# Optimization experiments

Measured on AMD Instinct MI355X. Metric: run time of the kernel, lower is better.

## Reference

```python
import jax, jax.numpy as jnp
import numpy as np

N = 100000   # nodes
E = 1600000  # edges (before self-loops)
F = 128      # num_features
H = 128      # hidden_dim
EPS = 1e-5   # BatchNorm eps


def setup_inputs() -> dict:
    key = jax.random.key(0)
    ks = jax.random.split(key, 8)
    x = jax.random.normal(ks[0], (N, F), dtype=jnp.float32)
    edge_index = jax.random.randint(ks[1], (2, E), 0, N, dtype=jnp.int64)

    def lin(k, din, dout):
        s = 1.0 / np.sqrt(din)
        kw, kb = jax.random.split(k)
        W = jax.random.uniform(kw, (din, dout), jnp.float32, -s, s)
        b = jax.random.uniform(kb, (dout,), jnp.float32, -s, s)
        return W, b

    W1, b1 = lin(ks[2], F, H)
    W2, b2 = lin(ks[3], H, H)
    W3, b3 = lin(ks[4], H, H)
    Wc, bc = lin(ks[5], H, 2)

    def bn_params():
        return (jnp.ones((H,), jnp.float32), jnp.zeros((H,), jnp.float32),
                jnp.zeros((H,), jnp.float32), jnp.ones((H,), jnp.float32))

    g1, be1, rm1, rv1 = bn_params()
    g2, be2, rm2, rv2 = bn_params()
    g3, be3, rm3, rv3 = bn_params()

    return {"x": x, "edge_index": edge_index,
            "W1": W1, "b1": b1, "W2": W2, "b2": b2, "W3": W3, "b3": b3,
            "g1": g1, "be1": be1, "rm1": rm1, "rv1": rv1,
            "g2": g2, "be2": be2, "rm2": rm2, "rv2": rv2,
            "g3": g3, "be3": be3, "rm3": rm3, "rv3": rv3,
            "Wc": Wc, "bc": bc}


def _gcn_norm(edge_index, num_nodes):
    # add self-loops, compute symmetric normalization (PyG GCNConv default)
    loop = jnp.arange(num_nodes, dtype=edge_index.dtype)
    src = jnp.concatenate([edge_index[0], loop])
    dst = jnp.concatenate([edge_index[1], loop])
    deg = jax.ops.segment_sum(jnp.ones_like(dst, dtype=jnp.float32), dst,
                              num_segments=num_nodes)
    dinv = jnp.where(deg > 0, jax.lax.rsqrt(deg), 0.0)
    norm = dinv[src] * dinv[dst]  # [E+N]
    return src, dst, norm


def _gcn_conv(x, W, b, src, dst, norm, num_nodes):
    h = x @ W                              # [N, H] linear first
    msg = h[src] * norm[:, None]           # gather + scale  [E+N, H]
    out = jax.ops.segment_sum(msg, dst, num_segments=num_nodes)  # scatter-add
    return out + b


def _bn_eval(x, g, be, rm, rv):
    return (x - rm) * jax.lax.rsqrt(rv + EPS) * g + be


def reference(x, edge_index,
              W1, b1, W2, b2, W3, b3,
              g1, be1, rm1, rv1,
              g2, be2, rm2, rv2,
              g3, be3, rm3, rv3,
              Wc, bc):
    n = x.shape[0]
    src, dst, norm = _gcn_norm(edge_index, n)
    h = _gcn_conv(x, W1, b1, src, dst, norm, n)
    h = _bn_eval(jax.nn.relu(h), g1, be1, rm1, rv1)
    # dropout: identity in eval mode
    h = _gcn_conv(h, W2, b2, src, dst, norm, n)
    h = _bn_eval(jax.nn.relu(h), g2, be2, rm2, rv2)
    h = _gcn_conv(h, W3, b3, src, dst, norm, n)
    h = _bn_eval(jax.nn.relu(h), g3, be3, rm3, rv3)
    return h @ Wc + bc  # [N, 2]
```

## Files before the change

### kernel.cpp

```cpp
#include <hip/hip_runtime.h>
#include <hip/hip_fp16.h>

#define BN_EPS 1e-5f
#define CHUNK 4096
#define BBITS 7

typedef _Float16 half8 __attribute__((ext_vector_type(8)));
typedef float f32x4 __attribute__((ext_vector_type(4)));

__device__ __forceinline__ float4 f4zero() { return make_float4(0.f, 0.f, 0.f, 0.f); }


__global__ __launch_bounds__(256) void k_pack_hist(const float* __restrict__ W1,
                                                   const float* __restrict__ W2,
                                                   const float* __restrict__ W3,
                                                   _Float16* __restrict__ pW,
                                                   const int* __restrict__ dst,
                                                   int* __restrict__ tableT,
                                                   int nA, int nbuck, int e) {
    __shared__ int h[1024];
    int tid = threadIdx.x;
    if (blockIdx.x < 24) {
        int t = blockIdx.x * 256 + tid;
        int wi = t >> 11;
        int tt = t & 2047;
        const float* W = (wi == 0) ? W1 : ((wi == 1) ? W2 : W3);
        int kc = tt >> 9;
        int rem = tt & 511;
        int ct = rem >> 6;
        int lane = rem & 63;
        int q = lane >> 4;
        int col = ct * 16 + (lane & 15);
        half8 hh;
#pragma unroll
        for (int j = 0; j < 8; ++j)
            hh[j] = (_Float16)W[(kc * 32 + q * 8 + j) * 128 + col];
        *(half8*)(pW + (size_t)t * 8) = hh;
        return;
    }
    int blk = blockIdx.x - 24;
    for (int k = tid; k < 1024; k += 256) h[k] = 0;
    __syncthreads();
    int base = blk * CHUNK;
    if (base + CHUNK <= e && (e & 3) == 0) {
        const int4* d4 = (const int4*)(dst + base);
#pragma unroll
        for (int t = 0; t < CHUNK / 1024; ++t) {
            int4 d = d4[t * 256 + tid];
            atomicAdd(&h[d.x >> BBITS], 1);
            atomicAdd(&h[d.y >> BBITS], 1);
            atomicAdd(&h[d.z >> BBITS], 1);
            atomicAdd(&h[d.w >> BBITS], 1);
        }
    } else {
        for (int i = base + tid; i < e && i < base + CHUNK; i += 256)
            atomicAdd(&h[dst[i] >> BBITS], 1);
    }
    __syncthreads();
    for (int k = tid; k < nbuck; k += 256)
        tableT[(size_t)k * nA + blk] = h[k];
}


__global__ __launch_bounds__(1024) void k_scan_block(const int* __restrict__ in,
                                                     int* __restrict__ outp,
                                                     int* __restrict__ partials, int len) {
    __shared__ int s[1024];
    int t = threadIdx.x;
    int gid = blockIdx.x * 1024 + t;
    int v = (gid < len) ? in[gid] : 0;
    int x = v;
    s[t] = x;
    __syncthreads();
    for (int d = 1; d < 1024; d <<= 1) {
        int y = (t >= d) ? s[t - d] : 0;
        __syncthreads();
        x += y;
        s[t] = x;
        __syncthreads();
    }
    if (gid < len) outp[gid] = x - v;
    if (t == 1023) partials[blockIdx.x] = x;
}

__global__ __launch_bounds__(256) void k_scan_addp(int* __restrict__ data,
                                                   const int* __restrict__ partials, int len) {
    __shared__ int red[256];
    int tid = threadIdx.x;
    int K = blockIdx.x >> 2;
    int s = 0;
    for (int t = tid; t < K; t += 256) s += partials[t];
    red[tid] = s;
    __syncthreads();
    for (int d = 128; d > 0; d >>= 1) {
        if (tid < d) red[tid] += red[tid + d];
        __syncthreads();
    }
    int gid = blockIdx.x * 256 + tid;
    if (gid < len) data[gid] += red[0];
}


template <bool AF32>
__device__ __forceinline__ void gemm_body(int bid, int tid, char* smem,
                                          const void* __restrict__ Av,
                                          const _Float16* __restrict__ pW,
                                          uint4* __restrict__ C, int n) {
    uint4* sW = (uint4*)smem;
    {
        const uint4* gW = (const uint4*)pW;
#pragma unroll
        for (int i = 0; i < 8; ++i) sW[tid + 256 * i] = gW[tid + 256 * i];
    }
    __syncthreads();

    int wave = tid >> 6, lane = tid & 63;
    int quad = lane >> 4, l16 = lane & 15;
    int row0 = bid * 64 + wave * 16;
    int arow = row0 + l16;
    int arowc = (arow < n) ? arow : (n - 1);

    half8 af[4];
    if (AF32) {
        const float* A = (const float*)Av + (size_t)arowc * 128 + quad * 8;
#pragma unroll
        for (int kc = 0; kc < 4; ++kc) {
            float4 lo = *(const float4*)(A + kc * 32);
            float4 hi = *(const float4*)(A + kc * 32 + 4);
            half8 h;
            h[0] = (_Float16)lo.x; h[1] = (_Float16)lo.y;
            h[2] = (_Float16)lo.z; h[3] = (_Float16)lo.w;
            h[4] = (_Float16)hi.x; h[5] = (_Float16)hi.y;
            h[6] = (_Float16)hi.z; h[7] = (_Float16)hi.w;
            af[kc] = h;
        }
    } else {
        const _Float16* A = (const _Float16*)Av + (size_t)arowc * 128 + quad * 8;
#pragma unroll
        for (int kc = 0; kc < 4; ++kc)
            af[kc] = *(const half8*)(A + kc * 32);
    }

    f32x4 acc[8];
#pragma unroll
    for (int ct = 0; ct < 8; ++ct) acc[ct] = (f32x4){0.f, 0.f, 0.f, 0.f};

#pragma unroll
    for (int kc = 0; kc < 4; ++kc) {
#pragma unroll
        for (int ct = 0; ct < 8; ++ct) {
            half8 bf = *(half8*)&sW[(kc * 8 + ct) * 64 + lane];
            acc[ct] = __builtin_amdgcn_mfma_f32_16x16x32_f16(af[kc], bf, acc[ct], 0, 0, 0);
        }
    }

    __syncthreads();

    _Float16* eb = (_Float16*)smem + wave * 16 * 136;
#pragma unroll
    for (int ct = 0; ct < 8; ++ct)
#pragma unroll
        for (int r = 0; r < 4; ++r)
            eb[(quad * 4 + r) * 136 + ct * 16 + l16] = (_Float16)(acc[ct][r]);

#pragma unroll
    for (int i = 0; i < 4; ++i) {
        int linear = i * 64 + lane;
        int r = linear >> 4, c = linear & 15;
        uint4 v = *(uint4*)((char*)eb + r * 272 + c * 16);
        int row = row0 + r;
        if (row < n) C[(size_t)row * 16 + c] = v;
    }
}

__global__ __launch_bounds__(256) void k_gemm_mfma(const void* __restrict__ Av,
                                                   const _Float16* __restrict__ pW,
                                                   uint4* __restrict__ C, int n) {
    __shared__ char smem[32768];
    gemm_body<false>(blockIdx.x, threadIdx.x, smem, Av, pW, C, n);
}


__global__ __launch_bounds__(256) void k_scatter_gemm(const int* __restrict__ src,
                                                      const int* __restrict__ dst,
                                                      const int* __restrict__ tableT,
                                                      int2* __restrict__ bed,
                                                      int nA, int nbuck, int e,
                                                      const float* __restrict__ x,
                                                      const _Float16* __restrict__ pW,
                                                      uint4* __restrict__ C, int n) {
    __shared__ char smem[32768];
    int tid = threadIdx.x;
    if ((int)blockIdx.x >= nA) {
        gemm_body<true>((int)blockIdx.x - nA, tid, smem, x, pW, C, n);
        return;
    }
    int* cur = (int*)smem;
    int blk = blockIdx.x;
    for (int k = tid; k < nbuck; k += 256)
        cur[k] = tableT[(size_t)k * nA + blk];
    __syncthreads();
    int base = blk * CHUNK;
    if (base + CHUNK <= e && (e & 3) == 0) {
        const int4* s4 = (const int4*)(src + base);
        const int4* d4 = (const int4*)(dst + base);
#pragma unroll
        for (int t = 0; t < CHUNK / 1024; ++t) {
            int4 s = s4[t * 256 + tid];
            int4 d = d4[t * 256 + tid];
            int p0 = atomicAdd(&cur[d.x >> BBITS], 1); bed[p0] = make_int2(s.x, d.x);
            int p1 = atomicAdd(&cur[d.y >> BBITS], 1); bed[p1] = make_int2(s.y, d.y);
            int p2 = atomicAdd(&cur[d.z >> BBITS], 1); bed[p2] = make_int2(s.z, d.z);
            int p3 = atomicAdd(&cur[d.w >> BBITS], 1); bed[p3] = make_int2(s.w, d.w);
        }
    } else {
        for (int i = base + tid; i < e && i < base + CHUNK; i += 256) {
            int d = dst[i];
            int p = atomicAdd(&cur[d >> BBITS], 1);
            bed[p] = make_int2(src[i], d);
        }
    }
}


__global__ __launch_bounds__(256) void k_rank_finalize(const int2* __restrict__ bed,
                                                       const int* __restrict__ tableT,
                                                       int2* __restrict__ offs2,
                                                       int* __restrict__ er,
                                                       float* __restrict__ dinv,
                                                       unsigned int* __restrict__ bufAzero,
                                                       int nA, int nbuck, int n, int e) {
    __shared__ int lcnt[128];
    __shared__ int lscan[128];
    __shared__ int loff[128];
    int b = blockIdx.x, tid = threadIdx.x;
    if (tid < 128) lcnt[tid] = 0;
    __syncthreads();
    int start = tableT[(size_t)b * nA];
    int end = (b + 1 < nbuck) ? tableT[(size_t)(b + 1) * nA] : e;
    for (int i = start + tid; i < end; i += 256)
        atomicAdd(&lcnt[bed[i].y & 127], 1);
    __syncthreads();
    int padded = 0;
    if (tid < 128) {
        padded = (lcnt[tid] + 7) & ~7;
        lscan[tid] = padded;
    }
    __syncthreads();
    for (int d = 1; d < 128; d <<= 1) {
        int y = (tid < 128 && tid >= d) ? lscan[tid - d] : 0;
        __syncthreads();
        if (tid < 128) lscan[tid] += y;
        __syncthreads();
    }
    int ebase = start + (b << 10);
    if (tid < 128) {
        loff[tid] = lscan[tid] - padded;
        int node = (b << BBITS) + tid;
        if (node < n) {
            int c = lcnt[tid];
            int o = ebase + loff[tid];
            offs2[node] = make_int2(o, o + padded);
            dinv[node] = rsqrtf((float)(c + 1));
            for (int j = c; j < padded; ++j) er[o + j] = n << 8;
        }
    }
    if (b == 0 && tid < 64) bufAzero[tid] = 0u;
    if (b == 0 && tid == 0) dinv[n] = 0.f;
    __syncthreads();
    if (tid < 128) lcnt[tid] = 0;
    __syncthreads();
    for (int i = start + tid; i < end; i += 256) {
        int2 q = bed[i];
        int l = q.y & 127;
        int r = atomicAdd(&lcnt[l], 1);
        er[ebase + loff[l] + r] = q.x << 8;
    }
}


__device__ __forceinline__ void acc_row4(float4& aL, float4& aH, uint4 q) {
    asm("v_fma_mix_f32 %0, %1, 1.0, %0 op_sel:[0,0,0] op_sel_hi:[1,0,0]" : "+v"(aL.x) : "v"(q.x));
    asm("v_fma_mix_f32 %0, %1, 1.0, %0 op_sel:[1,0,0] op_sel_hi:[1,0,0]" : "+v"(aL.y) : "v"(q.x));
    asm("v_fma_mix_f32 %0, %1, 1.0, %0 op_sel:[0,0,0] op_sel_hi:[1,0,0]" : "+v"(aL.z) : "v"(q.y));
    asm("v_fma_mix_f32 %0, %1, 1.0, %0 op_sel:[1,0,0] op_sel_hi:[1,0,0]" : "+v"(aL.w) : "v"(q.y));
    asm("v_fma_mix_f32 %0, %1, 1.0, %0 op_sel:[0,0,0] op_sel_hi:[1,0,0]" : "+v"(aH.x) : "v"(q.z));
    asm("v_fma_mix_f32 %0, %1, 1.0, %0 op_sel:[1,0,0] op_sel_hi:[1,0,0]" : "+v"(aH.y) : "v"(q.z));
    asm("v_fma_mix_f32 %0, %1, 1.0, %0 op_sel:[0,0,0] op_sel_hi:[1,0,0]" : "+v"(aH.z) : "v"(q.w));
    asm("v_fma_mix_f32 %0, %1, 1.0, %0 op_sel:[1,0,0] op_sel_hi:[1,0,0]" : "+v"(aH.w) : "v"(q.w));
}

__device__ __forceinline__ void acc_row4s(float4& aL, float4& aH, uint4 q, float s) {
    asm("v_fma_mix_f32 %0, %1, %2, %0 op_sel:[0,0,0] op_sel_hi:[1,0,0]" : "+v"(aL.x) : "v"(q.x), "v"(s));
    asm("v_fma_mix_f32 %0, %1, %2, %0 op_sel:[1,0,0] op_sel_hi:[1,0,0]" : "+v"(aL.y) : "v"(q.x), "v"(s));
    asm("v_fma_mix_f32 %0, %1, %2, %0 op_sel:[0,0,0] op_sel_hi:[1,0,0]" : "+v"(aL.z) : "v"(q.y), "v"(s));
    asm("v_fma_mix_f32 %0, %1, %2, %0 op_sel:[1,0,0] op_sel_hi:[1,0,0]" : "+v"(aL.w) : "v"(q.y), "v"(s));
    asm("v_fma_mix_f32 %0, %1, %2, %0 op_sel:[0,0,0] op_sel_hi:[1,0,0]" : "+v"(aH.x) : "v"(q.z), "v"(s));
    asm("v_fma_mix_f32 %0, %1, %2, %0 op_sel:[1,0,0] op_sel_hi:[1,0,0]" : "+v"(aH.y) : "v"(q.z), "v"(s));
    asm("v_fma_mix_f32 %0, %1, %2, %0 op_sel:[0,0,0] op_sel_hi:[1,0,0]" : "+v"(aH.z) : "v"(q.w), "v"(s));
    asm("v_fma_mix_f32 %0, %1, %2, %0 op_sel:[1,0,0] op_sel_hi:[1,0,0]" : "+v"(aH.w) : "v"(q.w), "v"(s));
}


template <bool FUSE_CLS, bool SRC_SCALE>
__global__ __launch_bounds__(256) void k_aggregate(const uint4* __restrict__ Ah,
                                                   const int2* __restrict__ offs2,
                                                   const int* __restrict__ er,
                                                   const float* __restrict__ dinv,
                                                   const float* __restrict__ bias,
                                                   const float* __restrict__ g,
                                                   const float* __restrict__ be,
                                                   const float* __restrict__ rm,
                                                   const float* __restrict__ rv,
                                                   uint4* __restrict__ Hout,
                                                   const float* __restrict__ Wc,
                                                   const float* __restrict__ bc,
                                                   float* __restrict__ out, int n) {
    int lane = threadIdx.x & 15;
    int node = blockIdx.x * 16 + (threadIdx.x >> 4);
    if (node >= n) return;

    const char* AhB = (const char*)Ah;
    unsigned int l16 = (unsigned int)lane * 16u;

    float di = dinv[node];
    float4 aL = f4zero(), aH = f4zero();
    {
        uint4 qs = *(const uint4*)(AhB + (((unsigned int)node << 8) + l16));
        if (SRC_SCALE) acc_row4s(aL, aH, qs, di);
        else           acc_row4(aL, aH, qs);
    }

    int2 offc = offs2[node];
    int e0 = offc.x, e1 = offc.y;
    for (int e = e0; e < e1; e += 8) {
        int4 ra = *(const int4*)(er + e);
        int4 rb = *(const int4*)(er + e + 4);
        uint4 v0 = *(const uint4*)(AhB + ((unsigned int)ra.x + l16));
        uint4 v1 = *(const uint4*)(AhB + ((unsigned int)ra.y + l16));
        uint4 v2 = *(const uint4*)(AhB + ((unsigned int)ra.z + l16));
        uint4 v3 = *(const uint4*)(AhB + ((unsigned int)ra.w + l16));
        uint4 v4 = *(const uint4*)(AhB + ((unsigned int)rb.x + l16));
        uint4 v5 = *(const uint4*)(AhB + ((unsigned int)rb.y + l16));
        uint4 v6 = *(const uint4*)(AhB + ((unsigned int)rb.z + l16));
        uint4 v7 = *(const uint4*)(AhB + ((unsigned int)rb.w + l16));
        if (SRC_SCALE) {
            float d0 = dinv[(unsigned int)ra.x >> 8];
            float d1 = dinv[(unsigned int)ra.y >> 8];
            float d2 = dinv[(unsigned int)ra.z >> 8];
            float d3 = dinv[(unsigned int)ra.w >> 8];
            float d4 = dinv[(unsigned int)rb.x >> 8];
            float d5 = dinv[(unsigned int)rb.y >> 8];
            float d6 = dinv[(unsigned int)rb.z >> 8];
            float d7 = dinv[(unsigned int)rb.w >> 8];
            acc_row4s(aL, aH, v0, d0); acc_row4s(aL, aH, v1, d1);
            acc_row4s(aL, aH, v2, d2); acc_row4s(aL, aH, v3, d3);
            acc_row4s(aL, aH, v4, d4); acc_row4s(aL, aH, v5, d5);
            acc_row4s(aL, aH, v6, d6); acc_row4s(aL, aH, v7, d7);
        } else {
            acc_row4(aL, aH, v0); acc_row4(aL, aH, v1); acc_row4(aL, aH, v2); acc_row4(aL, aH, v3);
            acc_row4(aL, aH, v4); acc_row4(aL, aH, v5); acc_row4(aL, aH, v6); acc_row4(aL, aH, v7);
        }
    }

    aL.x *= di; aL.y *= di; aL.z *= di; aL.w *= di;
    aH.x *= di; aH.y *= di; aH.z *= di; aH.w *= di;

    float4 bL  = ((const float4*)bias)[2 * lane], bH  = ((const float4*)bias)[2 * lane + 1];
    float4 gL  = ((const float4*)g)[2 * lane],    gH  = ((const float4*)g)[2 * lane + 1];
    float4 beL = ((const float4*)be)[2 * lane],   beH = ((const float4*)be)[2 * lane + 1];
    float4 rmL = ((const float4*)rm)[2 * lane],   rmH = ((const float4*)rm)[2 * lane + 1];
    float4 rvL = ((const float4*)rv)[2 * lane],   rvH = ((const float4*)rv)[2 * lane + 1];

    float4 oL, oH;
    float v;
    v = fmaxf(aL.x + bL.x, 0.f); oL.x = (v - rmL.x) * rsqrtf(rvL.x + BN_EPS) * gL.x + beL.x;
    v = fmaxf(aL.y + bL.y, 0.f); oL.y = (v - rmL.y) * rsqrtf(rvL.y + BN_EPS) * gL.y + beL.y;
    v = fmaxf(aL.z + bL.z, 0.f); oL.z = (v - rmL.z) * rsqrtf(rvL.z + BN_EPS) * gL.z + beL.z;
    v = fmaxf(aL.w + bL.w, 0.f); oL.w = (v - rmL.w) * rsqrtf(rvL.w + BN_EPS) * gL.w + beL.w;
    v = fmaxf(aH.x + bH.x, 0.f); oH.x = (v - rmH.x) * rsqrtf(rvH.x + BN_EPS) * gH.x + beH.x;
    v = fmaxf(aH.y + bH.y, 0.f); oH.y = (v - rmH.y) * rsqrtf(rvH.y + BN_EPS) * gH.y + beH.y;
    v = fmaxf(aH.z + bH.z, 0.f); oH.z = (v - rmH.z) * rsqrtf(rvH.z + BN_EPS) * gH.z + beH.z;
    v = fmaxf(aH.w + bH.w, 0.f); oH.w = (v - rmH.w) * rsqrtf(rvH.w + BN_EPS) * gH.w + beH.w;

    if (!FUSE_CLS) {
        __half2 p0 = __floats2half2_rn(oL.x, oL.y);
        __half2 p1 = __floats2half2_rn(oL.z, oL.w);
        __half2 p2 = __floats2half2_rn(oH.x, oH.y);
        __half2 p3 = __floats2half2_rn(oH.z, oH.w);
        uint4 u;
        u.x = *(unsigned int*)&p0;
        u.y = *(unsigned int*)&p1;
        u.z = *(unsigned int*)&p2;
        u.w = *(unsigned int*)&p3;
        Hout[(size_t)node * 16 + lane] = u;
    } else {
        const float4* Wv = (const float4*)Wc;
        float4 w0 = Wv[4 * lane];
        float4 w1 = Wv[4 * lane + 1];
        float4 w2 = Wv[4 * lane + 2];
        float4 w3 = Wv[4 * lane + 3];
        float p0 = oL.x * w0.x + oL.y * w0.z + oL.z * w1.x + oL.w * w1.z
                 + oH.x * w2.x + oH.y * w2.z + oH.z * w3.x + oH.w * w3.z;
        float p1 = oL.x * w0.y + oL.y * w0.w + oL.z * w1.y + oL.w * w1.w
                 + oH.x * w2.y + oH.y * w2.w + oH.z * w3.y + oH.w * w3.w;
#pragma unroll
        for (int d = 8; d >= 1; d >>= 1) {
            p0 += __shfl_down(p0, d, 16);
            p1 += __shfl_down(p1, d, 16);
        }
        if (lane == 0) {
            out[node * 2 + 0] = p0 + bc[0];
            out[node * 2 + 1] = p1 + bc[1];
        }
    }
}


extern "C" void kernel_launch(void* const* d_in, const int* in_sizes, int n_in,
                              void* d_out, int out_size, void* d_ws, size_t ws_size,
                              hipStream_t stream) {
    const float* x   = (const float*)d_in[0];
    const int*   ei  = (const int*)d_in[1];
    const float* W1  = (const float*)d_in[2];
    const float* b1  = (const float*)d_in[3];
    const float* W2  = (const float*)d_in[4];
    const float* b2  = (const float*)d_in[5];
    const float* W3  = (const float*)d_in[6];
    const float* b3  = (const float*)d_in[7];
    const float* g1  = (const float*)d_in[8];
    const float* be1 = (const float*)d_in[9];
    const float* rm1 = (const float*)d_in[10];
    const float* rv1 = (const float*)d_in[11];
    const float* g2  = (const float*)d_in[12];
    const float* be2 = (const float*)d_in[13];
    const float* rm2 = (const float*)d_in[14];
    const float* rv2 = (const float*)d_in[15];
    const float* g3  = (const float*)d_in[16];
    const float* be3 = (const float*)d_in[17];
    const float* rm3 = (const float*)d_in[18];
    const float* rv3 = (const float*)d_in[19];
    const float* Wc  = (const float*)d_in[20];
    const float* bc  = (const float*)d_in[21];
    float* out = (float*)d_out;

    int n = in_sizes[0] / 128;
    int e = in_sizes[1] / 2;
    const int* src = ei;
    const int* dst = ei + e;

    char* ws = (char*)d_ws;
    size_t off = 0;
    auto alloc = [&](size_t bytes) -> char* {
        char* p = ws + off;
        off += (bytes + 255) & ~(size_t)255;
        return p;
    };
    int nA    = (e + CHUNK - 1) / CHUNK;
    int nbuck = (n + (1 << BBITS) - 1) >> BBITS;
    int tlen  = nbuck * nA;
    int erCap = e + (nbuck << 10) + 64;

    char*      bufA     = (char*) alloc((size_t)(n + 1) * 256);
    char*      bufH     = (char*) alloc((size_t)n * 256);
    float*     dinv     = (float*)alloc((size_t)(n + 1) * 4);
    int2*      offs2    = (int2*) alloc((size_t)n * 8);
    int*       tableT   = (int*)  alloc((size_t)(tlen + 1) * 4);
    int*       parts    = (int*)  alloc(8192);
    int*       er       = (int*)  alloc((size_t)erCap * 4);
    _Float16*  pW       = (_Float16*)alloc(3 * 16384 * 2);
    (void)ws_size; (void)n_in; (void)out_size;

    int2* bed = (int2*)bufH;

    int nbT   = (tlen + 1023) / 1024;
    int gT    = (tlen + 255) / 256;
    int gGemm = (n + 63) / 64;
    int gAgg  = (n + 15) / 16;

    k_pack_hist<<<24 + nA, 256, 0, stream>>>(W1, W2, W3, pW, dst, tableT, nA, nbuck, e);
    k_scan_block<<<nbT, 1024, 0, stream>>>(tableT, tableT, parts, tlen);
    k_scan_addp<<<gT, 256, 0, stream>>>(tableT, parts, tlen);
    k_scatter_gemm<<<nA + gGemm, 256, 0, stream>>>(src, dst, tableT, bed, nA, nbuck, e,
                                                   x, pW, (uint4*)bufA, n);
    k_rank_finalize<<<nbuck, 256, 0, stream>>>(bed, tableT, offs2, er, dinv,
                                               (unsigned int*)(bufA + (size_t)n * 256),
                                               nA, nbuck, n, e);

    k_aggregate<false, true><<<gAgg, 256, 0, stream>>>((const uint4*)bufA, offs2, er, dinv,
                                                       b1, g1, be1, rm1, rv1, (uint4*)bufH,
                                                       nullptr, nullptr, nullptr, n);
    k_gemm_mfma<<<gGemm, 256, 0, stream>>>(bufH, pW + 16384, (uint4*)bufA, n);
    k_aggregate<false, true><<<gAgg, 256, 0, stream>>>((const uint4*)bufA, offs2, er, dinv,
                                                       b2, g2, be2, rm2, rv2, (uint4*)bufH,
                                                       nullptr, nullptr, nullptr, n);
    k_gemm_mfma<<<gGemm, 256, 0, stream>>>(bufH, pW + 32768, (uint4*)bufA, n);
    k_aggregate<true, true><<<gAgg, 256, 0, stream>>>((const uint4*)bufA, offs2, er, dinv,
                                                      b3, g3, be3, rm3, rv3, nullptr,
                                                      Wc, bc, out, n);
}
```

Measured before the change: 390.3 us.

## Fuse aggregation with next-layer GEMM via per-tile counters and restructure scatter

```diff
diff --git a/kernel.cpp b/kernel.cpp
--- a/kernel.cpp
+++ b/kernel.cpp
@@ -7,6 +7,7 @@
 
 typedef _Float16 half8 __attribute__((ext_vector_type(8)));
 typedef float f32x4 __attribute__((ext_vector_type(4)));
+typedef unsigned int u32x4 __attribute__((ext_vector_type(4)));
 
 __device__ __forceinline__ float4 f4zero() { return make_float4(0.f, 0.f, 0.f, 0.f); }
 
@@ -42,7 +43,7 @@
     for (int k = tid; k < 1024; k += 256) h[k] = 0;
     __syncthreads();
     int base = blk * CHUNK;
-    if (base + CHUNK <= e && (e & 3) == 0) {
+    if (base + CHUNK <= e) {
         const int4* d4 = (const int4*)(dst + base);
 #pragma unroll
         for (int t = 0; t < CHUNK / 1024; ++t) {
@@ -53,7 +54,7 @@
             atomicAdd(&h[d.w >> BBITS], 1);
         }
     } else {
-        for (int i = base + tid; i < e && i < base + CHUNK; i += 256)
+        for (int i = base + tid; i < e; i += 256)
             atomicAdd(&h[dst[i] >> BBITS], 1);
     }
     __syncthreads();
@@ -101,6 +102,34 @@
 }
 
 
+__global__ __launch_bounds__(1024) void k_scatter(const int* __restrict__ src,
+                                                  const int* __restrict__ dst,
+                                                  const int* __restrict__ tableT,
+                                                  int2* __restrict__ bed,
+                                                  int nA, int nbuck, int e) {
+    __shared__ int cur[1024];
+    int blk = blockIdx.x, tid = threadIdx.x;
+    for (int k = tid; k < nbuck; k += 1024)
+        cur[k] = tableT[(size_t)k * nA + blk];
+    __syncthreads();
+    int base = blk * CHUNK;
+    if (base + CHUNK <= e) {
+        int4 s = ((const int4*)(src + base))[tid];
+        int4 d = ((const int4*)(dst + base))[tid];
+        int p0 = atomicAdd(&cur[d.x >> BBITS], 1); bed[p0] = make_int2(s.x, d.x);
+        int p1 = atomicAdd(&cur[d.y >> BBITS], 1); bed[p1] = make_int2(s.y, d.y);
+        int p2 = atomicAdd(&cur[d.z >> BBITS], 1); bed[p2] = make_int2(s.z, d.z);
+        int p3 = atomicAdd(&cur[d.w >> BBITS], 1); bed[p3] = make_int2(s.w, d.w);
+    } else {
+        for (int i = base + tid; i < e; i += 1024) {
+            int d = dst[i];
+            int p = atomicAdd(&cur[d >> BBITS], 1);
+            bed[p] = make_int2(src[i], d);
+        }
+    }
+}
+
+
 template <bool AF32>
 __device__ __forceinline__ void gemm_body(int bid, int tid, char* smem,
                                           const void* __restrict__ Av,
@@ -173,67 +202,35 @@
     }
 }
 
-__global__ __launch_bounds__(256) void k_gemm_mfma(const void* __restrict__ Av,
-                                                   const _Float16* __restrict__ pW,
-                                                   uint4* __restrict__ C, int n) {
-    __shared__ char smem[32768];
-    gemm_body<false>(blockIdx.x, threadIdx.x, smem, Av, pW, C, n);
-}
-
-
-__global__ __launch_bounds__(256) void k_scatter_gemm(const int* __restrict__ src,
-                                                      const int* __restrict__ dst,
-                                                      const int* __restrict__ tableT,
-                                                      int2* __restrict__ bed,
-                                                      int nA, int nbuck, int e,
-                                                      const float* __restrict__ x,
-                                                      const _Float16* __restrict__ pW,
-                                                      uint4* __restrict__ C, int n) {
+
+__global__ __launch_bounds__(256) void k_rank_gemm1(const int2* __restrict__ bed,
+                                                    const int* __restrict__ tableT,
+                                                    int2* __restrict__ offs2,
+                                                    int* __restrict__ er,
+                                                    float* __restrict__ dinv,
+                                                    unsigned int* __restrict__ pad0,
+                                                    unsigned int* __restrict__ pad1,
+                                                    unsigned int* __restrict__ pad2,
+                                                    int* __restrict__ cntAll, int cntLen,
+                                                    const float* __restrict__ x,
+                                                    const _Float16* __restrict__ pW,
+                                                    uint4* __restrict__ C,
+                                                    int nA, int nbuck, int n, int e) {
     __shared__ char smem[32768];
     int tid = threadIdx.x;
-    if ((int)blockIdx.x >= nA) {
-        gemm_body<true>((int)blockIdx.x - nA, tid, smem, x, pW, C, n);
+    int b = blockIdx.x;
+    if (b >= nbuck) {
+        gemm_body<true>(b - nbuck, tid, smem, x, pW, C, n);
         return;
     }
-    int* cur = (int*)smem;
-    int blk = blockIdx.x;
-    for (int k = tid; k < nbuck; k += 256)
-        cur[k] = tableT[(size_t)k * nA + blk];
-    __syncthreads();
-    int base = blk * CHUNK;
-    if (base + CHUNK <= e && (e & 3) == 0) {
-        const int4* s4 = (const int4*)(src + base);
-        const int4* d4 = (const int4*)(dst + base);
-#pragma unroll
-        for (int t = 0; t < CHUNK / 1024; ++t) {
-            int4 s = s4[t * 256 + tid];
-            int4 d = d4[t * 256 + tid];
-            int p0 = atomicAdd(&cur[d.x >> BBITS], 1); bed[p0] = make_int2(s.x, d.x);
-            int p1 = atomicAdd(&cur[d.y >> BBITS], 1); bed[p1] = make_int2(s.y, d.y);
-            int p2 = atomicAdd(&cur[d.z >> BBITS], 1); bed[p2] = make_int2(s.z, d.z);
-            int p3 = atomicAdd(&cur[d.w >> BBITS], 1); bed[p3] = make_int2(s.w, d.w);
-        }
-    } else {
-        for (int i = base + tid; i < e && i < base + CHUNK; i += 256) {
-            int d = dst[i];
-            int p = atomicAdd(&cur[d >> BBITS], 1);
-            bed[p] = make_int2(src[i], d);
-        }
-    }
-}
-
-
-__global__ __launch_bounds__(256) void k_rank_finalize(const int2* __restrict__ bed,
-                                                       const int* __restrict__ tableT,
-                                                       int2* __restrict__ offs2,
-                                                       int* __restrict__ er,
-                                                       float* __restrict__ dinv,
-                                                       unsigned int* __restrict__ bufAzero,
-                                                       int nA, int nbuck, int n, int e) {
-    __shared__ int lcnt[128];
-    __shared__ int lscan[128];
-    __shared__ int loff[128];
-    int b = blockIdx.x, tid = threadIdx.x;
+    int* lcnt  = (int*)smem;
+    int* lscan = lcnt + 128;
+    int* loff  = lscan + 128;
+    { int ci = b * 256 + tid; if (ci < cntLen) cntAll[ci] = 0; }
+    if (b == 0) {
+        if (tid < 64) { pad0[tid] = 0u; pad1[tid] = 0u; pad2[tid] = 0u; }
+        if (tid == 0) dinv[n] = 0.f;
+    }
     if (tid < 128) lcnt[tid] = 0;
     __syncthreads();
     int start = tableT[(size_t)b * nA];
@@ -265,8 +262,6 @@
             for (int j = c; j < padded; ++j) er[o + j] = n << 8;
         }
     }
-    if (b == 0 && tid < 64) bufAzero[tid] = 0u;
-    if (b == 0 && tid == 0) dinv[n] = 0.f;
     __syncthreads();
     if (tid < 128) lcnt[tid] = 0;
     __syncthreads();
@@ -302,67 +297,205 @@
 }
 
 
-template <bool FUSE_CLS, bool SRC_SCALE>
-__global__ __launch_bounds__(256) void k_aggregate(const uint4* __restrict__ Ah,
-                                                   const int2* __restrict__ offs2,
-                                                   const int* __restrict__ er,
-                                                   const float* __restrict__ dinv,
-                                                   const float* __restrict__ bias,
-                                                   const float* __restrict__ g,
-                                                   const float* __restrict__ be,
-                                                   const float* __restrict__ rm,
-                                                   const float* __restrict__ rv,
-                                                   uint4* __restrict__ Hout,
-                                                   const float* __restrict__ Wc,
-                                                   const float* __restrict__ bc,
-                                                   float* __restrict__ out, int n) {
+template <bool SRC_SCALE>
+__global__ __launch_bounds__(256) void k_agg_gemm(const uint4* __restrict__ Ah,
+                                                  const int2* __restrict__ offs2,
+                                                  const int* __restrict__ er,
+                                                  const float* __restrict__ dinv,
+                                                  const float* __restrict__ bias,
+                                                  const float* __restrict__ g,
+                                                  const float* __restrict__ be,
+                                                  const float* __restrict__ rm,
+                                                  const float* __restrict__ rv,
+                                                  uint4* __restrict__ Hout,
+                                                  int* __restrict__ cnt,
+                                                  const _Float16* __restrict__ pW,
+                                                  uint4* __restrict__ Cout,
+                                                  int n, int gAgg) {
+    __shared__ _Float16 ebs[4 * 16 * 136];
+    int tid = threadIdx.x;
+    if ((int)blockIdx.x < gAgg) {
+        int lane = tid & 15;
+        int node = blockIdx.x * 16 + (tid >> 4);
+        if (node < n) {
+            const char* AhB = (const char*)Ah;
+            unsigned int l16b = (unsigned int)lane * 16u;
+            float di = dinv[node];
+            float4 aL = f4zero(), aH = f4zero();
+            {
+                uint4 qs = *(const uint4*)(AhB + (((unsigned int)node << 8) + l16b));
+                if (SRC_SCALE) acc_row4s(aL, aH, qs, di);
+                else           acc_row4(aL, aH, qs);
+            }
+            int2 offc = offs2[node];
+            for (int ee = offc.x; ee < offc.y; ee += 8) {
+                int4 ra = *(const int4*)(er + ee);
+                int4 rb = *(const int4*)(er + ee + 4);
+                uint4 v0 = *(const uint4*)(AhB + ((unsigned int)ra.x + l16b));
+                uint4 v1 = *(const uint4*)(AhB + ((unsigned int)ra.y + l16b));
+                uint4 v2 = *(const uint4*)(AhB + ((unsigned int)ra.z + l16b));
+                uint4 v3 = *(const uint4*)(AhB + ((unsigned int)ra.w + l16b));
+                uint4 v4 = *(const uint4*)(AhB + ((unsigned int)rb.x + l16b));
+                uint4 v5 = *(const uint4*)(AhB + ((unsigned int)rb.y + l16b));
+                uint4 v6 = *(const uint4*)(AhB + ((unsigned int)rb.z + l16b));
+                uint4 v7 = *(const uint4*)(AhB + ((unsigned int)rb.w + l16b));
+                if (SRC_SCALE) {
+                    float d0 = dinv[(unsigned int)ra.x >> 8];
+                    float d1 = dinv[(unsigned int)ra.y >> 8];
+                    float d2 = dinv[(unsigned int)ra.z >> 8];
+                    float d3 = dinv[(unsigned int)ra.w >> 8];
+                    float d4 = dinv[(unsigned int)rb.x >> 8];
+                    float d5 = dinv[(unsigned int)rb.y >> 8];
+                    float d6 = dinv[(unsigned int)rb.z >> 8];
+                    float d7 = dinv[(unsigned int)rb.w >> 8];
+                    acc_row4s(aL, aH, v0, d0); acc_row4s(aL, aH, v1, d1);
+                    acc_row4s(aL, aH, v2, d2); acc_row4s(aL, aH, v3, d3);
+                    acc_row4s(aL, aH, v4, d4); acc_row4s(aL, aH, v5, d5);
+                    acc_row4s(aL, aH, v6, d6); acc_row4s(aL, aH, v7, d7);
+                } else {
+                    acc_row4(aL, aH, v0); acc_row4(aL, aH, v1);
+                    acc_row4(aL, aH, v2); acc_row4(aL, aH, v3);
+                    acc_row4(aL, aH, v4); acc_row4(aL, aH, v5);
+                    acc_row4(aL, aH, v6); acc_row4(aL, aH, v7);
+                }
+            }
+            aL.x *= di; aL.y *= di; aL.z *= di; aL.w *= di;
+            aH.x *= di; aH.y *= di; aH.z *= di; aH.w *= di;
+
+            float4 bL  = ((const float4*)bias)[2 * lane], bH  = ((const float4*)bias)[2 * lane + 1];
+            float4 gL  = ((const float4*)g)[2 * lane],    gH  = ((const float4*)g)[2 * lane + 1];
+            float4 beL = ((const float4*)be)[2 * lane],   beH = ((const float4*)be)[2 * lane + 1];
+            float4 rmL = ((const float4*)rm)[2 * lane],   rmH = ((const float4*)rm)[2 * lane + 1];
+            float4 rvL = ((const float4*)rv)[2 * lane],   rvH = ((const float4*)rv)[2 * lane + 1];
+
+            float4 oL, oH;
+            float v;
+            v = fmaxf(aL.x + bL.x, 0.f); oL.x = (v - rmL.x) * rsqrtf(rvL.x + BN_EPS) * gL.x + beL.x;
+            v = fmaxf(aL.y + bL.y, 0.f); oL.y = (v - rmL.y) * rsqrtf(rvL.y + BN_EPS) * gL.y + beL.y;
+            v = fmaxf(aL.z + bL.z, 0.f); oL.z = (v - rmL.z) * rsqrtf(rvL.z + BN_EPS) * gL.z + beL.z;
+            v = fmaxf(aL.w + bL.w, 0.f); oL.w = (v - rmL.w) * rsqrtf(rvL.w + BN_EPS) * gL.w + beL.w;
+            v = fmaxf(aH.x + bH.x, 0.f); oH.x = (v - rmH.x) * rsqrtf(rvH.x + BN_EPS) * gH.x + beH.x;
+            v = fmaxf(aH.y + bH.y, 0.f); oH.y = (v - rmH.y) * rsqrtf(rvH.y + BN_EPS) * gH.y + beH.y;
+            v = fmaxf(aH.z + bH.z, 0.f); oH.z = (v - rmH.z) * rsqrtf(rvH.z + BN_EPS) * gH.z + beH.z;
+            v = fmaxf(aH.w + bH.w, 0.f); oH.w = (v - rmH.w) * rsqrtf(rvH.w + BN_EPS) * gH.w + beH.w;
+
+            __half2 p0 = __floats2half2_rn(oL.x, oL.y);
+            __half2 p1 = __floats2half2_rn(oL.z, oL.w);
+            __half2 p2 = __floats2half2_rn(oH.x, oH.y);
+            __half2 p3 = __floats2half2_rn(oH.z, oH.w);
+            u32x4 u;
+            u.x = *(unsigned int*)&p0;
+            u.y = *(unsigned int*)&p1;
+            u.z = *(unsigned int*)&p2;
+            u.w = *(unsigned int*)&p3;
+            const uint4* pp = Hout + (size_t)node * 16 + lane;
+            asm volatile("global_store_dwordx4 %0, %1, off sc0 sc1"
+                         :: "v"(pp), "v"(u) : "memory");
+        }
+        asm volatile("s_waitcnt vmcnt(0)" ::: "memory");
+        __syncthreads();
+        if (tid == 0) atomicAdd(&cnt[blockIdx.x >> 2], 1);
+        return;
+    }
+    int bid2 = (int)blockIdx.x - gAgg;
+    int wave = tid >> 6, lane = tid & 63;
+    int quad = lane >> 4, l16 = lane & 15;
+#pragma unroll 1
+    for (int half = 0; half < 2; ++half) {
+        int bid = bid2 * 2 + half;
+        if (bid * 64 >= n) break;
+        int rem = n - bid * 64;
+        int expct = (rem >= 64) ? 4 : ((rem + 15) >> 4);
+        if (tid == 0) {
+            while (atomicAdd(&cnt[bid], 0) < expct) __builtin_amdgcn_s_sleep(8);
+        }
+        __syncthreads();
+
+        int row0 = bid * 64 + wave * 16;
+        int arow = row0 + l16;
+        int arowc = (arow < n) ? arow : (n - 1);
+        const _Float16* A = (const _Float16*)Hout + (size_t)arowc * 128 + quad * 8;
+        half8 af[4];
+#pragma unroll
+        for (int kc = 0; kc < 4; ++kc)
+            af[kc] = *(const half8*)(A + kc * 32);
+
+        f32x4 acc[8];
+#pragma unroll
+        for (int ct = 0; ct < 8; ++ct) acc[ct] = (f32x4){0.f, 0.f, 0.f, 0.f};
+#pragma unroll
+        for (int kc = 0; kc < 4; ++kc) {
+#pragma unroll
+            for (int ct = 0; ct < 8; ++ct) {
+                half8 bf = *(const half8*)(pW + (size_t)((kc * 8 + ct) * 64 + lane) * 8);
+                acc[ct] = __builtin_amdgcn_mfma_f32_16x16x32_f16(af[kc], bf, acc[ct], 0, 0, 0);
+            }
+        }
+
+        _Float16* eb = ebs + wave * 16 * 136;
+        float dv[4];
+#pragma unroll
+        for (int r = 0; r < 4; ++r) {
+            int rr = row0 + quad * 4 + r;
+            dv[r] = dinv[(rr < n) ? rr : (n - 1)];
+        }
+#pragma unroll
+        for (int ct = 0; ct < 8; ++ct)
+#pragma unroll
+            for (int r = 0; r < 4; ++r)
+                eb[(quad * 4 + r) * 136 + ct * 16 + l16] = (_Float16)(acc[ct][r] * dv[r]);
+        __syncthreads();
+#pragma unroll
+        for (int i = 0; i < 4; ++i) {
+            int linear = i * 64 + lane;
+            int r = linear >> 4, c = linear & 15;
+            uint4 v = *(uint4*)((char*)eb + r * 272 + c * 16);
+            int row = row0 + r;
+            if (row < n) Cout[(size_t)row * 16 + c] = v;
+        }
+    }
+}
+
+
+__global__ __launch_bounds__(256) void k_agg_cls(const uint4* __restrict__ Ah,
+                                                 const int2* __restrict__ offs2,
+                                                 const int* __restrict__ er,
+                                                 const float* __restrict__ dinv,
+                                                 const float* __restrict__ bias,
+                                                 const float* __restrict__ g,
+                                                 const float* __restrict__ be,
+                                                 const float* __restrict__ rm,
+                                                 const float* __restrict__ rv,
+                                                 const float* __restrict__ Wc,
+                                                 const float* __restrict__ bc,
+                                                 float* __restrict__ out, int n) {
     int lane = threadIdx.x & 15;
     int node = blockIdx.x * 16 + (threadIdx.x >> 4);
     if (node >= n) return;
 
     const char* AhB = (const char*)Ah;
-    unsigned int l16 = (unsigned int)lane * 16u;
+    unsigned int l16b = (unsigned int)lane * 16u;
+
+    float4 aL = f4zero(), aH = f4zero();
+    acc_row4(aL, aH, *(const uint4*)(AhB + (((unsigned int)node << 8) + l16b)));
+
+    int2 offc = offs2[node];
+    for (int ee = offc.x; ee < offc.y; ee += 8) {
+        int4 ra = *(const int4*)(er + ee);
+        int4 rb = *(const int4*)(er + ee + 4);
+        uint4 v0 = *(const uint4*)(AhB + ((unsigned int)ra.x + l16b));
+        uint4 v1 = *(const uint4*)(AhB + ((unsigned int)ra.y + l16b));
+        uint4 v2 = *(const uint4*)(AhB + ((unsigned int)ra.z + l16b));
+        uint4 v3 = *(const uint4*)(AhB + ((unsigned int)ra.w + l16b));
+        uint4 v4 = *(const uint4*)(AhB + ((unsigned int)rb.x + l16b));
+        uint4 v5 = *(const uint4*)(AhB + ((unsigned int)rb.y + l16b));
+        uint4 v6 = *(const uint4*)(AhB + ((unsigned int)rb.z + l16b));
+        uint4 v7 = *(const uint4*)(AhB + ((unsigned int)rb.w + l16b));
+        acc_row4(aL, aH, v0); acc_row4(aL, aH, v1); acc_row4(aL, aH, v2); acc_row4(aL, aH, v3);
+        acc_row4(aL, aH, v4); acc_row4(aL, aH, v5); acc_row4(aL, aH, v6); acc_row4(aL, aH, v7);
+    }
 
     float di = dinv[node];
-    float4 aL = f4zero(), aH = f4zero();
-    {
-        uint4 qs = *(const uint4*)(AhB + (((unsigned int)node << 8) + l16));
-        if (SRC_SCALE) acc_row4s(aL, aH, qs, di);
-        else           acc_row4(aL, aH, qs);
-    }
-
-    int2 offc = offs2[node];
-    int e0 = offc.x, e1 = offc.y;
-    for (int e = e0; e < e1; e += 8) {
-        int4 ra = *(const int4*)(er + e);
-        int4 rb = *(const int4*)(er + e + 4);
-        uint4 v0 = *(const uint4*)(AhB + ((unsigned int)ra.x + l16));
-        uint4 v1 = *(const uint4*)(AhB + ((unsigned int)ra.y + l16));
-        uint4 v2 = *(const uint4*)(AhB + ((unsigned int)ra.z + l16));
-        uint4 v3 = *(const uint4*)(AhB + ((unsigned int)ra.w + l16));
-        uint4 v4 = *(const uint4*)(AhB + ((unsigned int)rb.x + l16));
-        uint4 v5 = *(const uint4*)(AhB + ((unsigned int)rb.y + l16));
-        uint4 v6 = *(const uint4*)(AhB + ((unsigned int)rb.z + l16));
-        uint4 v7 = *(const uint4*)(AhB + ((unsigned int)rb.w + l16));
-        if (SRC_SCALE) {
-            float d0 = dinv[(unsigned int)ra.x >> 8];
-            float d1 = dinv[(unsigned int)ra.y >> 8];
-            float d2 = dinv[(unsigned int)ra.z >> 8];
-            float d3 = dinv[(unsigned int)ra.w >> 8];
-            float d4 = dinv[(unsigned int)rb.x >> 8];
-            float d5 = dinv[(unsigned int)rb.y >> 8];
-            float d6 = dinv[(unsigned int)rb.z >> 8];
-            float d7 = dinv[(unsigned int)rb.w >> 8];
-            acc_row4s(aL, aH, v0, d0); acc_row4s(aL, aH, v1, d1);
-            acc_row4s(aL, aH, v2, d2); acc_row4s(aL, aH, v3, d3);
-            acc_row4s(aL, aH, v4, d4); acc_row4s(aL, aH, v5, d5);
-            acc_row4s(aL, aH, v6, d6); acc_row4s(aL, aH, v7, d7);
-        } else {
-            acc_row4(aL, aH, v0); acc_row4(aL, aH, v1); acc_row4(aL, aH, v2); acc_row4(aL, aH, v3);
-            acc_row4(aL, aH, v4); acc_row4(aL, aH, v5); acc_row4(aL, aH, v6); acc_row4(aL, aH, v7);
-        }
-    }
-
     aL.x *= di; aL.y *= di; aL.z *= di; aL.w *= di;
     aH.x *= di; aH.y *= di; aH.z *= di; aH.w *= di;
 
@@ -383,36 +516,23 @@
     v = fmaxf(aH.z + bH.z, 0.f); oH.z = (v - rmH.z) * rsqrtf(rvH.z + BN_EPS) * gH.z + beH.z;
     v = fmaxf(aH.w + bH.w, 0.f); oH.w = (v - rmH.w) * rsqrtf(rvH.w + BN_EPS) * gH.w + beH.w;
 
-    if (!FUSE_CLS) {
-        __half2 p0 = __floats2half2_rn(oL.x, oL.y);
-        __half2 p1 = __floats2half2_rn(oL.z, oL.w);
-        __half2 p2 = __floats2half2_rn(oH.x, oH.y);
-        __half2 p3 = __floats2half2_rn(oH.z, oH.w);
-        uint4 u;
-        u.x = *(unsigned int*)&p0;
-        u.y = *(unsigned int*)&p1;
-        u.z = *(unsigned int*)&p2;
-        u.w = *(unsigned int*)&p3;
-        Hout[(size_t)node * 16 + lane] = u;
-    } else {
-        const float4* Wv = (const float4*)Wc;
-        float4 w0 = Wv[4 * lane];
-        float4 w1 = Wv[4 * lane + 1];
-        float4 w2 = Wv[4 * lane + 2];
-        float4 w3 = Wv[4 * lane + 3];
-        float p0 = oL.x * w0.x + oL.y * w0.z + oL.z * w1.x + oL.w * w1.z
-                 + oH.x * w2.x + oH.y * w2.z + oH.z * w3.x + oH.w * w3.z;
-        float p1 = oL.x * w0.y + oL.y * w0.w + oL.z * w1.y + oL.w * w1.w
-                 + oH.x * w2.y + oH.y * w2.w + oH.z * w3.y + oH.w * w3.w;
-#pragma unroll
-        for (int d = 8; d >= 1; d >>= 1) {
-            p0 += __shfl_down(p0, d, 16);
-            p1 += __shfl_down(p1, d, 16);
-        }
-        if (lane == 0) {
-            out[node * 2 + 0] = p0 + bc[0];
-            out[node * 2 + 1] = p1 + bc[1];
-        }
+    const float4* Wv = (const float4*)Wc;
+    float4 w0 = Wv[4 * lane];
+    float4 w1 = Wv[4 * lane + 1];
+    float4 w2 = Wv[4 * lane + 2];
+    float4 w3 = Wv[4 * lane + 3];
+    float p0 = oL.x * w0.x + oL.y * w0.z + oL.z * w1.x + oL.w * w1.z
+             + oH.x * w2.x + oH.y * w2.z + oH.z * w3.x + oH.w * w3.z;
+    float p1 = oL.x * w0.y + oL.y * w0.w + oL.z * w1.y + oL.w * w1.w
+             + oH.x * w2.y + oH.y * w2.w + oH.z * w3.y + oH.w * w3.w;
+#pragma unroll
+    for (int d = 8; d >= 1; d >>= 1) {
+        p0 += __shfl_down(p0, d, 16);
+        p1 += __shfl_down(p1, d, 16);
+    }
+    if (lane == 0) {
+        out[node * 2 + 0] = p0 + bc[0];
+        out[node * 2 + 1] = p1 + bc[1];
     }
 }
 
@@ -460,42 +580,44 @@
     int nbuck = (n + (1 << BBITS) - 1) >> BBITS;
     int tlen  = nbuck * nA;
     int erCap = e + (nbuck << 10) + 64;
-
-    char*      bufA     = (char*) alloc((size_t)(n + 1) * 256);
-    char*      bufH     = (char*) alloc((size_t)n * 256);
+    int gAgg  = (n + 15) / 16;
+    int gGemm = (n + 63) / 64;
+    int gHalf = (n + 127) / 128;
+
+    char*      buf0     = (char*) alloc((size_t)(n + 1) * 256);
+    char*      buf1     = (char*) alloc((size_t)(n + 1) * 256);
+    char*      buf2     = (char*) alloc((size_t)(n + 1) * 256);
     float*     dinv     = (float*)alloc((size_t)(n + 1) * 4);
     int2*      offs2    = (int2*) alloc((size_t)n * 8);
     int*       tableT   = (int*)  alloc((size_t)(tlen + 1) * 4);
     int*       parts    = (int*)  alloc(8192);
     int*       er       = (int*)  alloc((size_t)erCap * 4);
     _Float16*  pW       = (_Float16*)alloc(3 * 16384 * 2);
+    int*       cntAll   = (int*)  alloc((size_t)2 * gGemm * 4);
     (void)ws_size; (void)n_in; (void)out_size;
 
-    int2* bed = (int2*)bufH;
-
-    int nbT   = (tlen + 1023) / 1024;
-    int gT    = (tlen + 255) / 256;
-    int gGemm = (n + 63) / 64;
-    int gAgg  = (n + 15) / 16;
+    int2* bed = (int2*)buf2;
+
+    int nbT = (tlen + 1023) / 1024;
+    int gT  = (tlen + 255) / 256;
 
     k_pack_hist<<<24 + nA, 256, 0, stream>>>(W1, W2, W3, pW, dst, tableT, nA, nbuck, e);
     k_scan_block<<<nbT, 1024, 0, stream>>>(tableT, tableT, parts, tlen);
     k_scan_addp<<<gT, 256, 0, stream>>>(tableT, parts, tlen);
-    k_scatter_gemm<<<nA + gGemm, 256, 0, stream>>>(src, dst, tableT, bed, nA, nbuck, e,
-                                                   x, pW, (uint4*)bufA, n);
-    k_rank_finalize<<<nbuck, 256, 0, stream>>>(bed, tableT, offs2, er, dinv,
-                                               (unsigned int*)(bufA + (size_t)n * 256),
-                                               nA, nbuck, n, e);
-
-    k_aggregate<false, true><<<gAgg, 256, 0, stream>>>((const uint4*)bufA, offs2, er, dinv,
-                                                       b1, g1, be1, rm1, rv1, (uint4*)bufH,
-                                                       nullptr, nullptr, nullptr, n);
-    k_gemm_mfma<<<gGemm, 256, 0, stream>>>(bufH, pW + 16384, (uint4*)bufA, n);
-    k_aggregate<false, true><<<gAgg, 256, 0, stream>>>((const uint4*)bufA, offs2, er, dinv,
-                                                       b2, g2, be2, rm2, rv2, (uint4*)bufH,
-                                                       nullptr, nullptr, nullptr, n);
-    k_gemm_mfma<<<gGemm, 256, 0, stream>>>(bufH, pW + 32768, (uint4*)bufA, n);
-    k_aggregate<true, true><<<gAgg, 256, 0, stream>>>((const uint4*)bufA, offs2, er, dinv,
-                                                      b3, g3, be3, rm3, rv3, nullptr,
-                                                      Wc, bc, out, n);
-}
+    k_scatter<<<nA, 1024, 0, stream>>>(src, dst, tableT, bed, nA, nbuck, e);
+    k_rank_gemm1<<<nbuck + gGemm, 256, 0, stream>>>(
+        bed, tableT, offs2, er, dinv,
+        (unsigned int*)(buf0 + (size_t)n * 256),
+        (unsigned int*)(buf1 + (size_t)n * 256),
+        (unsigned int*)(buf2 + (size_t)n * 256),
+        cntAll, 2 * gGemm, x, pW, (uint4*)buf0, nA, nbuck, n, e);
+
+    k_agg_gemm<true><<<gAgg + gHalf, 256, 0, stream>>>(
+        (const uint4*)buf0, offs2, er, dinv, b1, g1, be1, rm1, rv1,
+        (uint4*)buf1, cntAll, pW + 16384, (uint4*)buf2, n, gAgg);
+    k_agg_gemm<false><<<gAgg + gHalf, 256, 0, stream>>>(
+        (const uint4*)buf2, offs2, er, dinv, b2, g2, be2, rm2, rv2,
+        (uint4*)buf0, cntAll + gGemm, pW + 32768, (uint4*)buf1, n, gAgg);
+    k_agg_cls<<<gAgg, 256, 0, stream>>>((const uint4*)buf1, offs2, er, dinv,
+                                        b3, g3, be3, rm3, rv3, Wc, bc, out, n);
+}
```

Measured after the change: 379.9 us. 2.7% less time.
